# Performance work log

Measured on AMD Instinct MI355X. Metric: run time of the kernel, lower is better.

## Reference

```python
import jax, jax.numpy as jnp
import numpy as np

B_SZ, L, N, H = 8, 4096, 256, 256
R_MIN, R_MAX, MAX_PHASE = 0.0, 1.0, 0.314


def setup_inputs() -> dict:
    key = jax.random.key(0)
    ks = jax.random.split(key, 8)
    x = jax.random.normal(ks[0], (B_SZ, L, H), jnp.float32)
    def glorot(k, shape):
        return jax.random.normal(k, shape, jnp.float32) * jnp.sqrt(2.0 / (shape[0] + shape[1])).astype(jnp.float32)
    B_re = glorot(ks[1], (N, H))
    B_im = glorot(ks[2], (N, H))
    C_re = glorot(ks[3], (H, N))
    C_im = glorot(ks[4], (H, N))
    # DiskRingRadius / DiskRingPhase initializers
    u1 = jax.random.uniform(ks[5], (N,), jnp.float32, 1e-6, 1.0)
    u2 = jax.random.uniform(ks[6], (N,), jnp.float32, 1e-6, 1.0)
    nu_log = jnp.log(-0.5 * jnp.log(u1 * (R_MAX ** 2 - R_MIN ** 2) + R_MIN ** 2))
    theta_log = jnp.log(MAX_PHASE * u2)
    D = jax.random.normal(ks[7], (H,), jnp.float32) * 0.05  # RandomNormal(stddev=0.05)
    return dict(x=x, B_re=B_re, B_im=B_im, C_re=C_re, C_im=C_im,
                nu_log=nu_log, theta_log=theta_log, D=D)


def reference(x, B_re, B_im, C_re, C_im, nu_log, theta_log, D):
    # Diagonal complex recurrence parameters
    Lambda = jnp.exp(jax.lax.complex(-jnp.exp(nu_log), jnp.exp(theta_log)))  # [N]
    gamma = jnp.sqrt(1.0 - jnp.abs(Lambda) ** 2).astype(jnp.complex64)       # [N]
    B_norm = (B_re + 1j * B_im).astype(jnp.complex64) * gamma[:, None]       # [N,H]
    C = (C_re + 1j * C_im).astype(jnp.complex64)                             # [H,N]

    # Input projection: [B,L,N] complex
    Bu = jnp.einsum('blh,nh->bln', x.astype(jnp.complex64), B_norm)
    Lambda_el = jnp.broadcast_to(Lambda, Bu.shape)

    def combine(a, b):
        la, ba = a
        lb, bb = b
        return (la * lb, lb * ba + bb)

    _, states = jax.lax.associative_scan(combine, (Lambda_el, Bu), axis=1)  # [B,L,N]

    y = jnp.real(jnp.einsum('bln,hn->blh', states, C))
    y = y + x * D  # H_in == H -> elementwise skip
    return y
```

## Files before the change

kernel.cpp:

```cpp
#include <hip/hip_runtime.h>
#include <hip/hip_bf16.h>
#include <math.h>

#define B_SZ 8
#define LSEQ 4096
#define NDIM 256
#define HDIM 256
#define MROWS (B_SZ * LSEQ)
#define CH 64
#define NC (LSEQ / CH)

#define BM 64
#define BN 128
#define BK 32
#define SSTR 68

typedef _Float16 half8 __attribute__((ext_vector_type(8)));
typedef _Float16 half4 __attribute__((ext_vector_type(4)));
typedef float fx4 __attribute__((ext_vector_type(4)));

__global__ void k_prep(const float* __restrict__ Bre, const float* __restrict__ Bim,
                       const float* __restrict__ Cre, const float* __restrict__ Cim,
                       const float* __restrict__ nu_log, const float* __restrict__ th_log,
                       _Float16* __restrict__ BreH, _Float16* __restrict__ BimH,
                       _Float16* __restrict__ CreH, _Float16* __restrict__ CimNH,
                       float* __restrict__ lamRe, float* __restrict__ lamIm,
                       float* __restrict__ powRe, float* __restrict__ powIm) {
    int r = blockIdx.x;
    int t = threadIdx.x;
    float nu  = expf(nu_log[r]);
    float th  = expf(th_log[r]);
    float mod = expf(-nu);
    float g   = sqrtf(fmaxf(1.0f - mod * mod, 0.0f));
    if (t == 0) {
        lamRe[r] = mod * cosf(th);
        lamIm[r] = mod * sinf(th);
    }
    int i = r * 256 + t;
    BreH[i]  = (_Float16)(Bre[i] * g);
    BimH[i]  = (_Float16)(Bim[i] * g);
    CreH[i]  = (_Float16)Cre[i];
    CimNH[i] = (_Float16)(-Cim[i]);
    if (r < CH) {
        float nuN = expf(nu_log[t]);
        float thN = expf(th_log[t]);
        float k   = (float)(r + 1);
        float mo  = expf(-nuN * k);
        powRe[r * 256 + t] = mo * cosf(thN * k);
        powIm[r * 256 + t] = mo * sinf(thN * k);
    }
}

__launch_bounds__(256)
__global__ void k_buscan(const float* __restrict__ x,
                         const _Float16* __restrict__ BreH,
                         const _Float16* __restrict__ BimH,
                         const float* __restrict__ lamRe,
                         const float* __restrict__ lamIm,
                         _Float16* __restrict__ stReH,
                         _Float16* __restrict__ stImH,
                         float* __restrict__ finRe,
                         float* __restrict__ finIm) {
    __shared__ __align__(16) _Float16 smem[20480];

    const int tid  = threadIdx.x;
    const int lane = tid & 63;
    const int wave = tid >> 6;
    const int wr   = wave >> 1;
    const int wc   = wave & 1;
    const int m0   = blockIdx.x * BM;
    const int n0   = blockIdx.y * BN;

    const int ar = tid >> 2, ac = (tid & 3) * 8;
    const int aw = ar * 32 + (((tid & 3) ^ ((tid >> 3) & 3)) * 8);

    const int br = tid >> 1, g2 = tid & 1, bc = g2 * 16;
    const int fb = (br >> 1) & 3;
    const int bw0 = br * 32 + (((2 * g2)     ^ fb) * 8);
    const int bw1 = br * 32 + (((2 * g2 + 1) ^ fb) * 8);

    const int fRC   = lane & 15;
    const int rslot = (((lane >> 4) ^ (fRC >> 1)) & 3) * 8;

    fx4 accR[8], accI[8];
#pragma unroll
    for (int i = 0; i < 8; ++i) { accR[i] = (fx4)0.0f; accI[i] = (fx4)0.0f; }

    float4 xf0, xf1;
    half8 w0, w1, w2, w3;

#define LOAD_T(K0)                                                          \
    {                                                                       \
        const float* xp = x + (size_t)(m0 + ar) * HDIM + (K0) + ac;         \
        xf0 = *(const float4*)xp;                                           \
        xf1 = *(const float4*)(xp + 4);                                     \
        const _Float16* bp1 = BreH + (size_t)(n0 + br) * HDIM + (K0) + bc;  \
        const _Float16* bp2 = BimH + (size_t)(n0 + br) * HDIM + (K0) + bc;  \
        w0 = *(const half8*)bp1;  w1 = *(const half8*)(bp1 + 8);            \
        w2 = *(const half8*)bp2;  w3 = *(const half8*)(bp2 + 8);            \
    }
#define WRITE_T(PO)                                                         \
    {                                                                       \
        half8 hv;                                                           \
        hv[0]=(_Float16)xf0.x; hv[1]=(_Float16)xf0.y; hv[2]=(_Float16)xf0.z; hv[3]=(_Float16)xf0.w; \
        hv[4]=(_Float16)xf1.x; hv[5]=(_Float16)xf1.y; hv[6]=(_Float16)xf1.z; hv[7]=(_Float16)xf1.w; \
        *(half8*)&smem[(PO) + aw] = hv;                                     \
        *(half8*)&smem[(PO) + 2048 + bw0] = w0;                             \
        *(half8*)&smem[(PO) + 2048 + bw1] = w1;                             \
        *(half8*)&smem[(PO) + 6144 + bw0] = w2;                             \
        *(half8*)&smem[(PO) + 6144 + bw1] = w3;                             \
    }

    LOAD_T(0);
    WRITE_T(0);
    __syncthreads();

    int p = 0;
    for (int k0 = 0; k0 < HDIM; k0 += BK) {
        const int po = p * 10240;
        const int qo = (p ^ 1) * 10240;
        const bool nx = (k0 + BK) < HDIM;
        if (nx) LOAD_T(k0 + BK);
        half8 af[2], bf[4];
#pragma unroll
        for (int sm = 0; sm < 2; ++sm)
            af[sm] = *(const half8*)&smem[po + (wr * 32 + sm * 16 + fRC) * 32 + rslot];
#pragma unroll
        for (int sn = 0; sn < 4; ++sn)
            bf[sn] = *(const half8*)&smem[po + 2048 + (wc * 64 + sn * 16 + fRC) * 32 + rslot];
#pragma unroll
        for (int sm = 0; sm < 2; ++sm)
#pragma unroll
            for (int sn = 0; sn < 4; ++sn)
                accR[sm * 4 + sn] = __builtin_amdgcn_mfma_f32_16x16x32_f16(af[sm], bf[sn], accR[sm * 4 + sn], 0, 0, 0);
#pragma unroll
        for (int sn = 0; sn < 4; ++sn)
            bf[sn] = *(const half8*)&smem[po + 6144 + (wc * 64 + sn * 16 + fRC) * 32 + rslot];
#pragma unroll
        for (int sm = 0; sm < 2; ++sm)
#pragma unroll
            for (int sn = 0; sn < 4; ++sn)
                accI[sm * 4 + sn] = __builtin_amdgcn_mfma_f32_16x16x32_f16(af[sm], bf[sn], accI[sm * 4 + sn], 0, 0, 0);
        if (nx) WRITE_T(qo);
        __syncthreads();
        p ^= 1;
    }
#undef LOAD_T
#undef WRITE_T

    _Float16* SRe = smem;
    _Float16* SIm = smem + 8704;

    const int rBase = (lane >> 4) * 4;
#pragma unroll
    for (int sm = 0; sm < 2; ++sm)
#pragma unroll
        for (int sn = 0; sn < 4; ++sn) {
            int col = wc * 64 + sn * 16 + fRC;
            int row = wr * 32 + sm * 16 + rBase;
            half4 h1, h2;
#pragma unroll
            for (int reg = 0; reg < 4; ++reg) {
                h1[reg] = (_Float16)accR[sm * 4 + sn][reg];
                h2[reg] = (_Float16)accI[sm * 4 + sn][reg];
            }
            *(half4*)&SRe[col * SSTR + row] = h1;
            *(half4*)&SIm[col * SSTR + row] = h2;
        }
    __syncthreads();

    if (tid < BN) {
        int col = tid;
        int n = n0 + col;
        float lr = lamRe[n], li = lamIm[n];
        _Float16* cR = &SRe[col * SSTR];
        _Float16* cI = &SIm[col * SSTR];
        float sr = 0.0f, si = 0.0f;
#pragma unroll 8
        for (int r = 0; r < CH; ++r) {
            float ur = (float)cR[r];
            float ui = (float)cI[r];
            float nr = fmaf(lr, sr, fmaf(-li, si, ur));
            float ni = fmaf(lr, si, fmaf(li, sr, ui));
            sr = nr; si = ni;
            cR[r] = (_Float16)sr;
            cI[r] = (_Float16)si;
        }
        int bb = blockIdx.x >> 6, cc = blockIdx.x & 63;
        size_t f = ((size_t)(bb * NC + cc)) * NDIM + n;
        finRe[f] = sr;
        finIm[f] = si;
    }
    __syncthreads();

    {
        int row = tid >> 2;
        int cb  = (tid & 3) * 8;
        size_t gbase = (size_t)(m0 + row) * NDIM + n0 + cb;
#pragma unroll
        for (int g = 0; g < 4; ++g) {
            half8 h1, h2;
#pragma unroll
            for (int e = 0; e < 8; ++e) {
                int col = cb + g * 32 + e;
                h1[e] = SRe[col * SSTR + row];
                h2[e] = SIm[col * SSTR + row];
            }
            *(half8*)(stReH + gbase + g * 32) = h1;
            *(half8*)(stImH + gbase + g * 32) = h2;
        }
    }
}

__launch_bounds__(256)
__global__ void k_carry(const float* __restrict__ lamRe,
                        const float* __restrict__ lamIm,
                        const float* __restrict__ finRe,
                        const float* __restrict__ finIm,
                        float* __restrict__ carRe,
                        float* __restrict__ carIm) {
    const int tid  = threadIdx.x;
    const int lane = tid & 63;
    const int wv   = tid >> 6;
    const int idx  = blockIdx.x * 4 + wv;
    const int b    = idx >> 8;
    const int n    = idx & 255;

    float plr = lamRe[n], pli = lamIm[n];
#pragma unroll
    for (int i = 0; i < 6; ++i) {
        float t = plr * plr - pli * pli;
        pli = 2.0f * plr * pli;
        plr = t;
    }

    size_t base = ((size_t)(b * NC + lane)) * NDIM + n;
    float vr = finRe[base];
    float vi = finIm[base];

#pragma unroll
    for (int d = 1; d < 64; d <<= 1) {
        float vpr = __shfl_up(vr, d);
        float vpi = __shfl_up(vi, d);
        float lpr = __shfl_up(plr, d);
        float lpi = __shfl_up(pli, d);
        if (lane >= d) {
            float nvr = fmaf(plr, vpr, fmaf(-pli, vpi, vr));
            float nvi = fmaf(plr, vpi, fmaf(pli, vpr, vi));
            vr = nvr; vi = nvi;
            float t = plr * lpr - pli * lpi;
            pli = fmaf(plr, lpi, pli * lpr);
            plr = t;
        }
    }

    float cr = __shfl_up(vr, 1);
    float ci = __shfl_up(vi, 1);
    if (lane == 0) { cr = 0.0f; ci = 0.0f; }
    carRe[base] = cr;
    carIm[base] = ci;
}

__launch_bounds__(256)
__global__ void k_out(const _Float16* __restrict__ sReH,
                      const _Float16* __restrict__ sImH,
                      const _Float16* __restrict__ CreH,
                      const _Float16* __restrict__ CimNH,
                      const float* __restrict__ powRe,
                      const float* __restrict__ powIm,
                      const float* __restrict__ carRe,
                      const float* __restrict__ carIm,
                      const float* __restrict__ x,
                      const float* __restrict__ Dv,
                      float* __restrict__ y) {
    __shared__ __align__(16) _Float16 sA1[2][2048];
    __shared__ __align__(16) _Float16 sA2[2][2048];
    __shared__ __align__(16) _Float16 sCr[2][4096];
    __shared__ __align__(16) _Float16 sCi[2][4096];

    const int tid  = threadIdx.x;
    const int lane = tid & 63;
    const int wave = tid >> 6;
    const int wr   = wave >> 1;
    const int wc   = wave & 1;
    const int m0   = blockIdx.x * BM;
    const int h0   = blockIdx.y * BN;
    const int chunk = m0 >> 6;

    const int ar = tid >> 2, ac = (tid & 3) * 8;
    const int aw = ar * 32 + (((tid & 3) ^ ((tid >> 3) & 3)) * 8);

    const int br = tid >> 1, g2 = tid & 1, bc = g2 * 16;
    const int fb = (br >> 1) & 3;
    const int bw0 = br * 32 + (((2 * g2)     ^ fb) * 8);
    const int bw1 = br * 32 + (((2 * g2 + 1) ^ fb) * 8);

    const int fRC   = lane & 15;
    const int rslot = (((lane >> 4) ^ (fRC >> 1)) & 3) * 8;

    fx4 acc[8];
#pragma unroll
    for (int i = 0; i < 8; ++i) acc[i] = (fx4)0.0f;

    half8 s1, s2, c0a, c0b, c1a, c1b;
    float4 pr0, pr1, pi0, pi1, cr0, cr1, ci0, ci1;

#define LOAD_T(K0)                                                          \
    {                                                                       \
        size_t aOff = (size_t)(m0 + ar) * NDIM + (K0) + ac;                 \
        s1 = *(const half8*)(sReH + aOff);                                  \
        s2 = *(const half8*)(sImH + aOff);                                  \
        size_t pOff = (size_t)ar * NDIM + (K0) + ac;                        \
        pr0 = *(const float4*)(powRe + pOff); pr1 = *(const float4*)(powRe + pOff + 4); \
        pi0 = *(const float4*)(powIm + pOff); pi1 = *(const float4*)(powIm + pOff + 4); \
        size_t cOff = (size_t)chunk * NDIM + (K0) + ac;                     \
        cr0 = *(const float4*)(carRe + cOff); cr1 = *(const float4*)(carRe + cOff + 4); \
        ci0 = *(const float4*)(carIm + cOff); ci1 = *(const float4*)(carIm + cOff + 4); \
        const _Float16* cp1 = CreH  + (size_t)(h0 + br) * NDIM + (K0) + bc; \
        const _Float16* cp2 = CimNH + (size_t)(h0 + br) * NDIM + (K0) + bc; \
        c0a = *(const half8*)cp1;  c0b = *(const half8*)(cp1 + 8);          \
        c1a = *(const half8*)cp2;  c1b = *(const half8*)(cp2 + 8);          \
    }
#define WRITE_T(PB)                                                         \
    {                                                                       \
        float prA[8] = {pr0.x,pr0.y,pr0.z,pr0.w,pr1.x,pr1.y,pr1.z,pr1.w};   \
        float piA[8] = {pi0.x,pi0.y,pi0.z,pi0.w,pi1.x,pi1.y,pi1.z,pi1.w};   \
        float crA[8] = {cr0.x,cr0.y,cr0.z,cr0.w,cr1.x,cr1.y,cr1.z,cr1.w};   \
        float ciA[8] = {ci0.x,ci0.y,ci0.z,ci0.w,ci1.x,ci1.y,ci1.z,ci1.w};   \
        half8 h1, h2;                                                       \
        _Pragma("unroll")                                                   \
        for (int e = 0; e < 8; ++e) {                                       \
            float ur = fmaf(prA[e], crA[e], fmaf(-piA[e], ciA[e], (float)s1[e])); \
            float ui = fmaf(prA[e], ciA[e], fmaf( piA[e], crA[e], (float)s2[e])); \
            h1[e] = (_Float16)ur; h2[e] = (_Float16)ui;                     \
        }                                                                   \
        *(half8*)&sA1[PB][aw] = h1;                                         \
        *(half8*)&sA2[PB][aw] = h2;                                         \
        *(half8*)&sCr[PB][bw0] = c0a;  *(half8*)&sCr[PB][bw1] = c0b;        \
        *(half8*)&sCi[PB][bw0] = c1a;  *(half8*)&sCi[PB][bw1] = c1b;        \
    }

    LOAD_T(0);
    WRITE_T(0);
    __syncthreads();

    int p = 0;
    for (int k0 = 0; k0 < NDIM; k0 += BK) {
        const bool nx = (k0 + BK) < NDIM;
        if (nx) LOAD_T(k0 + BK);
        half8 af[2], bf[4];
#pragma unroll
        for (int sm = 0; sm < 2; ++sm)
            af[sm] = *(const half8*)&sA1[p][(wr * 32 + sm * 16 + fRC) * 32 + rslot];
#pragma unroll
        for (int sn = 0; sn < 4; ++sn)
            bf[sn] = *(const half8*)&sCr[p][(wc * 64 + sn * 16 + fRC) * 32 + rslot];
#pragma unroll
        for (int sm = 0; sm < 2; ++sm)
#pragma unroll
            for (int sn = 0; sn < 4; ++sn)
                acc[sm * 4 + sn] = __builtin_amdgcn_mfma_f32_16x16x32_f16(af[sm], bf[sn], acc[sm * 4 + sn], 0, 0, 0);
#pragma unroll
        for (int sm = 0; sm < 2; ++sm)
            af[sm] = *(const half8*)&sA2[p][(wr * 32 + sm * 16 + fRC) * 32 + rslot];
#pragma unroll
        for (int sn = 0; sn < 4; ++sn)
            bf[sn] = *(const half8*)&sCi[p][(wc * 64 + sn * 16 + fRC) * 32 + rslot];
#pragma unroll
        for (int sm = 0; sm < 2; ++sm)
#pragma unroll
            for (int sn = 0; sn < 4; ++sn)
                acc[sm * 4 + sn] = __builtin_amdgcn_mfma_f32_16x16x32_f16(af[sm], bf[sn], acc[sm * 4 + sn], 0, 0, 0);
        if (nx) WRITE_T(p ^ 1);
        __syncthreads();
        p ^= 1;
    }
#undef LOAD_T
#undef WRITE_T

    float d[4];
#pragma unroll
    for (int sn = 0; sn < 4; ++sn) d[sn] = Dv[h0 + wc * 64 + sn * 16 + fRC];

    const int rBase = (lane >> 4) * 4;
#pragma unroll
    for (int sm = 0; sm < 2; ++sm)
#pragma unroll
        for (int sn = 0; sn < 4; ++sn) {
            int h = h0 + wc * 64 + sn * 16 + fRC;
#pragma unroll
            for (int reg = 0; reg < 4; ++reg) {
                int m = m0 + wr * 32 + sm * 16 + rBase + reg;
                size_t idx = (size_t)m * HDIM + h;
                y[idx] = fmaf(x[idx], d[sn], acc[sm * 4 + sn][reg]);
            }
        }
}

extern "C" void kernel_launch(void* const* d_in, const int* in_sizes, int n_in,
                              void* d_out, int out_size, void* d_ws, size_t ws_size,
                              hipStream_t stream) {
    const float* x      = (const float*)d_in[0];
    const float* B_re   = (const float*)d_in[1];
    const float* B_im   = (const float*)d_in[2];
    const float* C_re   = (const float*)d_in[3];
    const float* C_im   = (const float*)d_in[4];
    const float* nu_log = (const float*)d_in[5];
    const float* th_log = (const float*)d_in[6];
    const float* D      = (const float*)d_in[7];
    float* y = (float*)d_out;

    char* p = (char*)d_ws;
    _Float16* stReH = (_Float16*)p;  p += (size_t)MROWS * NDIM * 2;
    _Float16* stImH = (_Float16*)p;  p += (size_t)MROWS * NDIM * 2;
    _Float16* BreH  = (_Float16*)p;  p += (size_t)NDIM * HDIM * 2;
    _Float16* BimH  = (_Float16*)p;  p += (size_t)NDIM * HDIM * 2;
    _Float16* CreH  = (_Float16*)p;  p += (size_t)HDIM * NDIM * 2;
    _Float16* CimNH = (_Float16*)p;  p += (size_t)HDIM * NDIM * 2;
    float* lamRe = (float*)p;  p += NDIM * 4;
    float* lamIm = (float*)p;  p += NDIM * 4;
    float* powRe = (float*)p;  p += (size_t)CH * NDIM * 4;
    float* powIm = (float*)p;  p += (size_t)CH * NDIM * 4;
    float* finRe = (float*)p;  p += (size_t)B_SZ * NC * NDIM * 4;
    float* finIm = (float*)p;  p += (size_t)B_SZ * NC * NDIM * 4;
    float* carRe = (float*)p;  p += (size_t)B_SZ * NC * NDIM * 4;
    float* carIm = (float*)p;  p += (size_t)B_SZ * NC * NDIM * 4;

    k_prep<<<NDIM, 256, 0, stream>>>(B_re, B_im, C_re, C_im, nu_log, th_log,
                                     BreH, BimH, CreH, CimNH, lamRe, lamIm,
                                     powRe, powIm);

    dim3 gGemm(MROWS / BM, NDIM / BN);
    k_buscan<<<gGemm, 256, 0, stream>>>(x, BreH, BimH, lamRe, lamIm,
                                        stReH, stImH, finRe, finIm);

    k_carry<<<(B_SZ * NDIM) / 4, 256, 0, stream>>>(lamRe, lamIm, finRe, finIm,
                                                   carRe, carIm);

    dim3 gOut(MROWS / BM, HDIM / BN);
    k_out<<<gOut, 256, 0, stream>>>(stReH, stImH, CreH, CimNH,
                                    powRe, powIm, carRe, carIm, x, D, y);
}
```

Measured before the change: 150.9 us.

## Widen buscan block to cover all N columns with 512 threads

The input-projection plus chunk-scan kernel now gives each 64-row tile a single block of 512 threads that covers all 256 state columns, where before two 256-thread blocks each handled 128 columns. The x tile is loaded and converted to half once per row tile instead of twice, and the grid is halved. In exchange shared memory per block nearly doubles and the launch-bounds hint changes, which may lower occupancy. Only half the threads (256) run the serial scan.

```diff
diff --git a/kernel.cpp b/kernel.cpp
--- a/kernel.cpp
+++ b/kernel.cpp
@@ -51,7 +51,7 @@
     }
 }
 
-__launch_bounds__(256)
+__launch_bounds__(512, 4)
 __global__ void k_buscan(const float* __restrict__ x,
                          const _Float16* __restrict__ BreH,
                          const _Float16* __restrict__ BimH,
@@ -61,18 +61,18 @@
                          _Float16* __restrict__ stImH,
                          float* __restrict__ finRe,
                          float* __restrict__ finIm) {
-    __shared__ __align__(16) _Float16 smem[20480];
+    __shared__ __align__(16) _Float16 smem[36864];
 
     const int tid  = threadIdx.x;
     const int lane = tid & 63;
     const int wave = tid >> 6;
-    const int wr   = wave >> 1;
-    const int wc   = wave & 1;
+    const int wr   = wave >> 2;
+    const int wc   = wave & 3;
     const int m0   = blockIdx.x * BM;
-    const int n0   = blockIdx.y * BN;
-
-    const int ar = tid >> 2, ac = (tid & 3) * 8;
-    const int aw = ar * 32 + (((tid & 3) ^ ((tid >> 3) & 3)) * 8);
+
+    const int ar = tid >> 3;
+    const int ac = (tid & 7) * 4;
+    const int aw = ar * 32 + ((((tid >> 1) & 3) ^ ((tid >> 4) & 3)) * 8) + (tid & 1) * 4;
 
     const int br = tid >> 1, g2 = tid & 1, bc = g2 * 16;
     const int fb = (br >> 1) & 3;
@@ -86,29 +86,28 @@
 #pragma unroll
     for (int i = 0; i < 8; ++i) { accR[i] = (fx4)0.0f; accI[i] = (fx4)0.0f; }
 
-    float4 xf0, xf1;
+    float4 xf0;
     half8 w0, w1, w2, w3;
 
 #define LOAD_T(K0)                                                          \
     {                                                                       \
         const float* xp = x + (size_t)(m0 + ar) * HDIM + (K0) + ac;         \
         xf0 = *(const float4*)xp;                                           \
-        xf1 = *(const float4*)(xp + 4);                                     \
-        const _Float16* bp1 = BreH + (size_t)(n0 + br) * HDIM + (K0) + bc;  \
-        const _Float16* bp2 = BimH + (size_t)(n0 + br) * HDIM + (K0) + bc;  \
+        const _Float16* bp1 = BreH + (size_t)br * HDIM + (K0) + bc;         \
+        const _Float16* bp2 = BimH + (size_t)br * HDIM + (K0) + bc;         \
         w0 = *(const half8*)bp1;  w1 = *(const half8*)(bp1 + 8);            \
         w2 = *(const half8*)bp2;  w3 = *(const half8*)(bp2 + 8);            \
     }
 #define WRITE_T(PO)                                                         \
     {                                                                       \
-        half8 hv;                                                           \
-        hv[0]=(_Float16)xf0.x; hv[1]=(_Float16)xf0.y; hv[2]=(_Float16)xf0.z; hv[3]=(_Float16)xf0.w; \
-        hv[4]=(_Float16)xf1.x; hv[5]=(_Float16)xf1.y; hv[6]=(_Float16)xf1.z; hv[7]=(_Float16)xf1.w; \
-        *(half8*)&smem[(PO) + aw] = hv;                                     \
-        *(half8*)&smem[(PO) + 2048 + bw0] = w0;                             \
-        *(half8*)&smem[(PO) + 2048 + bw1] = w1;                             \
-        *(half8*)&smem[(PO) + 6144 + bw0] = w2;                             \
-        *(half8*)&smem[(PO) + 6144 + bw1] = w3;                             \
+        half4 hv;                                                           \
+        hv[0]=(_Float16)xf0.x; hv[1]=(_Float16)xf0.y;                       \
+        hv[2]=(_Float16)xf0.z; hv[3]=(_Float16)xf0.w;                       \
+        *(half4*)&smem[(PO) + aw] = hv;                                     \
+        *(half8*)&smem[(PO) + 2048 + bw0]  = w0;                            \
+        *(half8*)&smem[(PO) + 2048 + bw1]  = w1;                            \
+        *(half8*)&smem[(PO) + 10240 + bw0] = w2;                            \
+        *(half8*)&smem[(PO) + 10240 + bw1] = w3;                            \
     }
 
     LOAD_T(0);
@@ -117,8 +116,8 @@
 
     int p = 0;
     for (int k0 = 0; k0 < HDIM; k0 += BK) {
-        const int po = p * 10240;
-        const int qo = (p ^ 1) * 10240;
+        const int po = p * 18432;
+        const int qo = (p ^ 1) * 18432;
         const bool nx = (k0 + BK) < HDIM;
         if (nx) LOAD_T(k0 + BK);
         half8 af[2], bf[4];
@@ -135,7 +134,7 @@
                 accR[sm * 4 + sn] = __builtin_amdgcn_mfma_f32_16x16x32_f16(af[sm], bf[sn], accR[sm * 4 + sn], 0, 0, 0);
 #pragma unroll
         for (int sn = 0; sn < 4; ++sn)
-            bf[sn] = *(const half8*)&smem[po + 6144 + (wc * 64 + sn * 16 + fRC) * 32 + rslot];
+            bf[sn] = *(const half8*)&smem[po + 10240 + (wc * 64 + sn * 16 + fRC) * 32 + rslot];
 #pragma unroll
         for (int sm = 0; sm < 2; ++sm)
 #pragma unroll
@@ -149,7 +148,7 @@
 #undef WRITE_T
 
     _Float16* SRe = smem;
-    _Float16* SIm = smem + 8704;
+    _Float16* SIm = smem + 17408;
 
     const int rBase = (lane >> 4) * 4;
 #pragma unroll
@@ -169,9 +168,9 @@
         }
     __syncthreads();
 
-    if (tid < BN) {
+    if (tid < NDIM) {
         int col = tid;
-        int n = n0 + col;
+        int n = col;
         float lr = lamRe[n], li = lamIm[n];
         _Float16* cR = &SRe[col * SSTR];
         _Float16* cI = &SIm[col * SSTR];
@@ -194,20 +193,20 @@
     __syncthreads();
 
     {
-        int row = tid >> 2;
-        int cb  = (tid & 3) * 8;
-        size_t gbase = (size_t)(m0 + row) * NDIM + n0 + cb;
+        int row = tid >> 3;
+        int cb  = (tid & 7) * 8;
+        size_t gbase = (size_t)(m0 + row) * NDIM + cb;
 #pragma unroll
         for (int g = 0; g < 4; ++g) {
             half8 h1, h2;
 #pragma unroll
             for (int e = 0; e < 8; ++e) {
-                int col = cb + g * 32 + e;
+                int col = cb + g * 64 + e;
                 h1[e] = SRe[col * SSTR + row];
                 h2[e] = SIm[col * SSTR + row];
             }
-            *(half8*)(stReH + gbase + g * 32) = h1;
-            *(half8*)(stImH + gbase + g * 32) = h2;
+            *(half8*)(stReH + gbase + g * 64) = h1;
+            *(half8*)(stImH + gbase + g * 64) = h2;
         }
     }
 }
@@ -430,9 +429,8 @@
                                      BreH, BimH, CreH, CimNH, lamRe, lamIm,
                                      powRe, powIm);
 
-    dim3 gGemm(MROWS / BM, NDIM / BN);
-    k_buscan<<<gGemm, 256, 0, stream>>>(x, BreH, BimH, lamRe, lamIm,
-                                        stReH, stImH, finRe, finIm);
+    k_buscan<<<MROWS / BM, 512, 0, stream>>>(x, BreH, BimH, lamRe, lamIm,
+                                             stReH, stImH, finRe, finIm);
 
     k_carry<<<(B_SZ * NDIM) / 4, 256, 0, stream>>>(lamRe, lamIm, finRe, finIm,
                                                    carRe, carIm);
```

New measurement: 152.3 us. No clear change (+0.9%).
